# Performance work log

Measured on AMD Instinct MI355X. Metric: run time of the kernel, lower is better.

Reference implementation:

```python
import jax, jax.numpy as jnp
import numpy as np

B, L, H, N = 4, 4096, 1024, 16
EPS = 1e-6  # layer_norm_epsilon


def setup_inputs() -> dict:
    key = jax.random.key(0)
    ks = jax.random.split(key, 8)
    hidden_states = jax.random.normal(ks[0], (B, L, H), dtype=jnp.float32)
    attention_mask = jnp.ones((B, L), dtype=jnp.float32)
    norm_weight = jnp.ones((H,), dtype=jnp.float32)
    # S4D init: dt log-uniform in [1e-3, 1e-1]; S4D-Lin A init; random C, D
    dt_min, dt_max = 1e-3, 1e-1
    log_dt = jax.random.uniform(ks[1], (H,), dtype=jnp.float32) * (
        float(np.log(dt_max)) - float(np.log(dt_min))) + float(np.log(dt_min))
    log_A_real = jnp.log(0.5 * jnp.ones((H, N), dtype=jnp.float32))
    A_imag = jnp.broadcast_to(float(np.pi) * jnp.arange(N, dtype=jnp.float32), (H, N))
    C_real = jax.random.normal(ks[2], (H, N), dtype=jnp.float32) * (0.5 ** 0.5)
    C_imag = jax.random.normal(ks[3], (H, N), dtype=jnp.float32) * (0.5 ** 0.5)
    D = jax.random.normal(ks[4], (H,), dtype=jnp.float32)
    out_w = jax.random.normal(ks[5], (2 * H, H), dtype=jnp.float32) * 0.02  # 1x1 conv to 2H (GLU)
    out_b = jnp.zeros((2 * H,), dtype=jnp.float32)
    return dict(hidden_states=hidden_states, attention_mask=attention_mask,
                norm_weight=norm_weight, log_dt=log_dt, log_A_real=log_A_real,
                A_imag=A_imag, C_real=C_real, C_imag=C_imag, D=D,
                out_w=out_w, out_b=out_b)


def _s4d_kernel(log_dt, log_A_real, A_imag, C_real, C_imag, length):
    """Diagonal SSM convolution kernel k[h, l] (S4D ZOH discretization)."""
    dt = jnp.exp(log_dt)                                   # (H,)
    A = -jnp.exp(log_A_real) + 1j * A_imag                 # (H, N) complex64
    C = C_real + 1j * C_imag                               # (H, N)
    dtA = A * dt[:, None]                                  # (H, N)
    C_disc = C * (jnp.exp(dtA) - 1.0) / A                  # (H, N)
    vand = jnp.exp(dtA[:, :, None] * jnp.arange(length, dtype=jnp.float32))  # (H, N, L)
    k = 2.0 * jnp.einsum('hn,hnl->hl', C_disc, vand).real  # (H, L)
    return k.astype(jnp.float32)


def reference(hidden_states, attention_mask, norm_weight, log_dt, log_A_real,
              A_imag, C_real, C_imag, D, out_w, out_b):
    # LongT5LayerNorm: RMSNorm (no mean subtraction), variance in fp32
    var = jnp.mean(jnp.square(hidden_states.astype(jnp.float32)), axis=-1, keepdims=True)
    normed = hidden_states * jax.lax.rsqrt(var + EPS) * norm_weight  # (B, L, H)
    # mask padded positions, go to channel-major layout (B, H, L)
    u = (normed * attention_mask[..., None]).transpose(0, 2, 1)
    Lx = u.shape[-1]
    k = _s4d_kernel(log_dt, log_A_real, A_imag, C_real, C_imag, Lx)  # (H, L)
    # causal convolution via FFT of length 2L
    nfft = 2 * Lx
    k_f = jnp.fft.rfft(k, n=nfft)                 # (H, nfft//2+1)
    u_f = jnp.fft.rfft(u, n=nfft)                 # (B, H, nfft//2+1)
    y = jnp.fft.irfft(u_f * k_f, n=nfft)[..., :Lx]  # (B, H, L)
    y = y + u * D[:, None]                        # skip connection
    y = jax.nn.gelu(y, approximate=False)         # torch nn.GELU (exact)
    # output 1x1 conv to 2H, then GLU over the channel dim
    z = jnp.einsum('bhl,oh->bol', y, out_w) + out_b[:, None]
    a, b = jnp.split(z, 2, axis=1)
    ssm_out = (a * jax.nn.sigmoid(b)).transpose(0, 2, 1)  # (B, L, H)
    # residual + dropout (eval mode -> identity)
    return hidden_states + ssm_out
```

## Files before the change

### kernel.cpp

```cpp
#include <hip/hip_runtime.h>

#define B_   4
#define L_   4096
#define H_   1024
#define N_   16
#define CH_  64
#define NC_  (L_/CH_)
#define M_   (B_*L_)
#define O2_  (2*H_)
#define EPS_ 1e-6f

typedef __attribute__((ext_vector_type(4))) float  f32x4;
typedef __attribute__((ext_vector_type(8))) __bf16 bf16x8;

__device__ __forceinline__ unsigned short f2bf(float x) {
  union { float f; unsigned int u; } v; v.f = x;
  unsigned int r = v.u + 0x7FFFu + ((v.u >> 16) & 1u);
  return (unsigned short)(r >> 16);
}
__device__ __forceinline__ float bf2f(unsigned short x) {
  union { unsigned int u; float f; } v; v.u = ((unsigned int)x) << 16;
  return v.f;
}

__device__ __forceinline__ void async_copy16(const void* g, void* l) {
  __builtin_amdgcn_global_load_lds(
      (const __attribute__((address_space(1))) unsigned int*)g,
      (__attribute__((address_space(3))) unsigned int*)l, 16, 0, 0);
}

__global__ void k_prep(const float* __restrict__ log_dt,
                       const float* __restrict__ log_A_real,
                       const float* __restrict__ A_imag,
                       const float* __restrict__ C_real,
                       const float* __restrict__ C_imag,
                       const float* __restrict__ outw,
                       const float* __restrict__ outb,
                       float* __restrict__ wr,  float* __restrict__ wi,
                       float* __restrict__ c2r, float* __restrict__ c2i,
                       float* __restrict__ wpr, float* __restrict__ wpi,
                       unsigned short* __restrict__ Wbf,
                       float* __restrict__ bp) {
  int idx = blockIdx.x * 256 + threadIdx.x;
  int p = idx >> 10, hh = idx & (H_ - 1);
  size_t src = (size_t)((p >> 1) + (p & 1) * H_) * H_ + hh;
  Wbf[idx] = f2bf(outw[src]);
  if (idx < O2_) bp[idx] = outb[(idx >> 1) + (idx & 1) * H_];
  if (idx < H_ * N_) {
    int h = idx / N_, n = idx % N_;
    int hn = h * N_ + n;
    float dt  = expf(log_dt[h]);
    float Ar  = -expf(log_A_real[hn]);
    float Ai  = A_imag[hn];
    float dr  = Ar * dt, di = Ai * dt;
    float er  = expf(dr);
    float wrv = er * cosf(di), wiv = er * sinf(di);
    float e1r = wrv - 1.0f, e1i = wiv;
    float den = Ar * Ar + Ai * Ai;
    float qr  = (e1r * Ar + e1i * Ai) / den;
    float qi  = (e1i * Ar - e1r * Ai) / den;
    float Cr  = C_real[hn], Ci = C_imag[hn];
    float cdr = Cr * qr - Ci * qi;
    float cdi = Cr * qi + Ci * qr;
    float ep  = expf((float)CH_ * dr);
    int o = n * H_ + h;
    wr[o]  = wrv;  wi[o]  = wiv;
    c2r[o] = 2.0f * cdr; c2i[o] = 2.0f * cdi;
    wpr[o] = ep * cosf((float)CH_ * di);
    wpi[o] = ep * sinf((float)CH_ * di);
  }
}

__global__ __launch_bounds__(256) void k_scale(const float* __restrict__ hs,
                                               const float* __restrict__ mask,
                                               float* __restrict__ scale) {
  int m = blockIdx.x, tid = threadIdx.x;
  float4 v = reinterpret_cast<const float4*>(hs + (size_t)m * H_)[tid];
  float s = v.x * v.x + v.y * v.y + v.z * v.z + v.w * v.w;
  #pragma unroll
  for (int off = 32; off > 0; off >>= 1) s += __shfl_down(s, off, 64);
  __shared__ float ps[4];
  if ((tid & 63) == 0) ps[tid >> 6] = s;
  __syncthreads();
  if (tid == 0) {
    float var = (ps[0] + ps[1] + ps[2] + ps[3]) * (1.0f / H_);
    scale[m] = rsqrtf(var + EPS_) * mask[m];
  }
}

__global__ __launch_bounds__(256) void k_scan1(const float* __restrict__ hs,
                                               const float* __restrict__ nw,
                                               const float* __restrict__ scale,
                                               const float* __restrict__ wr_,
                                               const float* __restrict__ wi_,
                                               float* __restrict__ endr,
                                               float* __restrict__ endi,
                                               unsigned short* __restrict__ ubf) {
  int tid = threadIdx.x;
  int h = blockIdx.x * 256 + tid;
  int c = blockIdx.y, b = blockIdx.z;
  float wr[N_], wi[N_], xr[N_], xi[N_];
  #pragma unroll
  for (int n = 0; n < N_; n++) {
    wr[n] = wr_[n * H_ + h]; wi[n] = wi_[n * H_ + h];
    xr[n] = 0.f; xi[n] = 0.f;
  }
  float nwh = nw[h];
  int l0 = c * CH_;
  const float* scp = scale + (size_t)b * L_ + l0;
  const float* hp = hs + ((size_t)b * L_ + l0) * H_ + h;
  unsigned short* up = ubf + ((size_t)b * L_ + l0) * H_ + h;
  #pragma unroll 8
  for (int l = 0; l < CH_; l++) {
    float u = hp[(size_t)l * H_] * scp[l] * nwh;
    unsigned short ub = f2bf(u);
    up[(size_t)l * H_] = ub;
    u = bf2f(ub);
    #pragma unroll
    for (int n = 0; n < N_; n++) {
      float oxr = xr[n];
      xr[n] = fmaf(wr[n], oxr, fmaf(-wi[n], xi[n], u));
      xi[n] = fmaf(wr[n], xi[n], wi[n] * oxr);
    }
  }
  size_t base = (((size_t)b * NC_ + c) * N_) * H_ + h;
  #pragma unroll
  for (int n = 0; n < N_; n++) {
    endr[base + (size_t)n * H_] = xr[n];
    endi[base + (size_t)n * H_] = xi[n];
  }
}

__global__ __launch_bounds__(256) void k_carry(const float* __restrict__ wpr_,
                                               const float* __restrict__ wpi_,
                                               const float* __restrict__ endr,
                                               const float* __restrict__ endi,
                                               float* __restrict__ carr,
                                               float* __restrict__ cari) {
  int idx = blockIdx.x * 256 + threadIdx.x;
  int h = idx & (H_ - 1);
  int n = (idx >> 10) & (N_ - 1);
  int b = idx >> 14;
  float wprv = wpr_[n * H_ + h], wpiv = wpi_[n * H_ + h];
  float sr = 0.f, si = 0.f;
  size_t cstride = (size_t)N_ * H_;
  size_t base = ((size_t)b * NC_) * cstride + (size_t)n * H_ + h;
  for (int c = 0; c < NC_; c++, base += cstride) {
    carr[base] = sr; cari[base] = si;
    float er = endr[base], ei = endi[base];
    float osr = sr;
    sr = fmaf(wprv, osr,  fmaf(-wpiv, si, er));
    si = fmaf(wprv, si, fmaf(wpiv, osr, ei));
  }
}

__global__ __launch_bounds__(256) void k_scan2(const unsigned short* __restrict__ ubf,
                                               const float* __restrict__ wr_,
                                               const float* __restrict__ wi_,
                                               const float* __restrict__ c2r_,
                                               const float* __restrict__ c2i_,
                                               const float* __restrict__ Dp,
                                               const float* __restrict__ carr,
                                               const float* __restrict__ cari,
                                               unsigned short* __restrict__ ybf) {
  __shared__ __align__(16) unsigned short us[CH_ * 256];
  int tid = threadIdx.x;
  int hb = blockIdx.x;
  int c = blockIdx.y, b = blockIdx.z;
  int h = hb * 256 + tid;
  int l0 = c * CH_;
  const unsigned short* usrc = ubf + ((size_t)b * L_ + l0) * H_ + hb * 256;
  #pragma unroll
  for (int i = 0; i < 8; i++) {
    int g = i * 256 + tid;
    int l = g >> 5, hq = (g & 31) * 8;
    async_copy16(usrc + (size_t)l * H_ + hq, &us[g * 8]);
  }
  __syncthreads();

  float yacc[CH_];
  float Dh = Dp[h];
  #pragma unroll
  for (int l = 0; l < CH_; l++)
    yacc[l] = Dh * bf2f(us[l * 256 + tid]);

  size_t base = (((size_t)b * NC_ + c) * N_) * H_ + h;
  for (int n = 0; n < N_; n++) {
    float wrv = wr_[n * H_ + h],  wiv = wi_[n * H_ + h];
    float crv = c2r_[n * H_ + h], civ = c2i_[n * H_ + h];
    float xr = carr[base + (size_t)n * H_];
    float xi = cari[base + (size_t)n * H_];
    #pragma unroll
    for (int l = 0; l < CH_; l++) {
      float u = bf2f(us[l * 256 + tid]);
      float oxr = xr;
      xr = fmaf(wrv, oxr, fmaf(-wiv, xi, u));
      xi = fmaf(wrv, xi, wiv * oxr);
      yacc[l] = fmaf(crv, xr, fmaf(-civ, xi, yacc[l]));
    }
  }
  unsigned short* yp = ybf + ((size_t)b * L_ + l0) * H_ + h;
  #pragma unroll
  for (int l = 0; l < CH_; l++) {
    float yv = yacc[l];
    float g = 0.5f * yv * (1.0f + erff(yv * 0.70710678118654752f));
    yp[(size_t)l * H_] = f2bf(g);
  }
}

#define BM2 256
#define BN2 256
#define NT2 16
#define GST 132
#define GEMM_LDS 131072

#define STAGE_A(buf, half, kt) do { \
  async_copy16(Ag + (size_t)(bm + rp0 + ((half) << 6)) * H_ + (kt) * 64 + ca0, \
               sA + (buf) * 32768 + ((half) << 13) + tid * 16); \
  async_copy16(Ag + (size_t)(bm + rp1 + 64 + ((half) << 6)) * H_ + (kt) * 64 + ca1, \
               sA + (buf) * 32768 + ((half) << 13) + 16384 + tid * 16); \
} while (0)

#define STAGE_B(buf, eo, kt) do { \
  async_copy16(Bg + (size_t)(bn + ((rp0 >> 5) << 6) + (rp0 & 31) + ((eo) << 5)) * H_ + (kt) * 64 + ca0, \
               sB + (buf) * 32768 + ((rp0 >> 5) << 13) + ((rp0 & 31) << 7) + ((eo) << 12) + (q0 << 4)); \
  async_copy16(Bg + (size_t)(bn + ((rp1 >> 5) << 6) + (rp1 & 31) + ((eo) << 5)) * H_ + (kt) * 64 + ca1, \
               sB + (buf) * 32768 + ((rp1 >> 5) << 13) + ((rp1 & 31) << 7) + ((eo) << 12) + (q0 << 4)); \
} while (0)

#define VM4  asm volatile("s_waitcnt vmcnt(4)" ::: "memory")
#define NOVM do {} while (0)
#define NOLOAD do {} while (0)

#define LOAD_A(buf, mh) do { \
  _Pragma("unroll") \
  for (int m2 = 0; m2 < 4; m2++) { \
    _Pragma("unroll") \
    for (int kk = 0; kk < 2; kk++) \
      afr[m2][kk] = *reinterpret_cast<const bf16x8*>( \
          sA + (buf) * 32768 + (((wm << 7) + ((mh) << 6) + (m2 << 4)) << 7) + aoff[kk]); \
  } \
} while (0)

#define LOAD_B(buf, nh, dst) do { \
  _Pragma("unroll") \
  for (int n2 = 0; n2 < 2; n2++) { \
    _Pragma("unroll") \
    for (int kk = 0; kk < 2; kk++) \
      dst[n2][kk] = *reinterpret_cast<const bf16x8*>( \
          sB + (buf) * 32768 + (((wn << 6) + ((nh) << 5) + (n2 << 4)) << 7) + aoff[kk]); \
  } \
} while (0)

#define PH(LOADS, STAGE_STMT, mh, nh, bfx, CLOSE_STMT) do { \
  LOADS; \
  STAGE_STMT; \
  asm volatile("" ::: "memory"); \
  __builtin_amdgcn_s_barrier(); \
  asm volatile("s_waitcnt lgkmcnt(0)" ::: "memory"); \
  __builtin_amdgcn_sched_barrier(0); \
  __builtin_amdgcn_s_setprio(1); \
  _Pragma("unroll") \
  for (int m2 = 0; m2 < 4; m2++) { \
    _Pragma("unroll") \
    for (int n2 = 0; n2 < 2; n2++) { \
      _Pragma("unroll") \
      for (int kk = 0; kk < 2; kk++) \
        acc[(mh) * 4 + m2][(nh) * 2 + n2] = __builtin_amdgcn_mfma_f32_16x16x32_bf16( \
            afr[m2][kk], bfx[n2][kk], acc[(mh) * 4 + m2][(nh) * 2 + n2], 0, 0, 0); \
    } \
  } \
  __builtin_amdgcn_s_setprio(0); \
  CLOSE_STMT; \
  asm volatile("" ::: "memory"); \
  __builtin_amdgcn_s_barrier(); \
  asm volatile("" ::: "memory"); \
} while (0)

__global__ __launch_bounds__(512, 2) void k_gemm(const unsigned short* __restrict__ Ag,
                                                 const unsigned short* __restrict__ Bg,
                                                 const float* __restrict__ bp,
                                                 const float* __restrict__ hs,
                                                 float* __restrict__ out) {
  extern __shared__ __align__(16) char smem[];
  char* sA = smem;
  char* sB = smem + 65536;
  const int tid  = threadIdx.x;
  const int lane = tid & 63;
  const int wave = tid >> 6;
  const int wm = wave >> 2;
  const int wn = wave & 3;
  const int lin = blockIdx.y * 8 + blockIdx.x;
  const int w   = ((lin & 7) << 6) + (lin >> 3);
  const int bn  = (w & 7) * BN2;
  const int bm  = (w >> 3) * BM2;
  const int ar = lane & 15, kqi = lane >> 4;

  const int rp0 = tid >> 3, q0 = tid & 7;
  const int rp1 = rp0 + 64;
  const int ca0 = (q0 ^ (rp0 & 7)) * 8;
  const int ca1 = (q0 ^ (rp1 & 7)) * 8;
  int aoff[2];
  #pragma unroll
  for (int kk = 0; kk < 2; kk++)
    aoff[kk] = ar * 128 + (((kk * 4 + kqi) ^ (ar & 7)) << 4);

  f32x4 acc[8][4];
  #pragma unroll
  for (int mi = 0; mi < 8; mi++)
    #pragma unroll
    for (int ni = 0; ni < 4; ni++) acc[mi][ni] = (f32x4){0.f, 0.f, 0.f, 0.f};

  bf16x8 afr[4][2], bf0[2][2], bf1[2][2];

  STAGE_A(0, 0, 0);
  STAGE_B(0, 0, 0);
  STAGE_A(0, 1, 0);
  STAGE_B(0, 1, 0);
  STAGE_A(1, 0, 1);
  STAGE_B(1, 1, 1);
  VM4;
  __builtin_amdgcn_s_barrier();
  asm volatile("" ::: "memory");

  #pragma unroll 1
  for (int i = 0; i < NT2 / 2; i++) {
    const int tb = 2 * i + 1;
    const int tc = (2 * i + 2 < NT2) ? 2 * i + 2 : NT2 - 1;
    const int td = (2 * i + 3 < NT2) ? 2 * i + 3 : NT2 - 1;
    PH(LOAD_A(0, 0); LOAD_B(0, 0, bf0), STAGE_A(1, 1, tb), 0, 0, bf0, NOVM);
    PH(LOAD_B(0, 1, bf1),               STAGE_B(1, 0, tb), 0, 1, bf1, NOVM);
    PH(LOAD_A(0, 1),                    STAGE_A(0, 0, tc), 1, 1, bf1, NOVM);
    PH(NOLOAD,                          STAGE_B(0, 1, tc), 1, 0, bf0, VM4);
    PH(LOAD_A(1, 0); LOAD_B(1, 0, bf0), STAGE_A(0, 1, tc), 0, 0, bf0, NOVM);
    PH(LOAD_B(1, 1, bf1),               STAGE_B(0, 0, tc), 0, 1, bf1, NOVM);
    PH(LOAD_A(1, 1),                    STAGE_A(1, 0, td), 1, 1, bf1, NOVM);
    PH(NOLOAD,                          STAGE_B(1, 1, td), 1, 0, bf0, VM4);
  }
  asm volatile("s_waitcnt vmcnt(0)" ::: "memory");
  __builtin_amdgcn_s_barrier();
  asm volatile("" ::: "memory");

  float* gt = (float*)smem;
  #pragma unroll
  for (int hf = 0; hf < 2; hf++) {
    if (wm == hf) {
      #pragma unroll
      for (int ni = 0; ni < 4; ni++) {
        int p  = wn * 64 + ni * 16 + (lane & 15);
        int pe = (bn + p) & ~1;
        float bA = bp[pe], bB = bp[pe + 1];
        int jl = p >> 1;
        #pragma unroll
        for (int mi = 0; mi < 8; mi++) {
          int lrow0 = mi * 16 + (lane >> 4) * 4;
          #pragma unroll
          for (int r = 0; r < 4; r++) {
            float v = acc[mi][ni][r];
            float w2 = __shfl_xor(v, 1, 64);
            if (!(lane & 1))
              gt[(lrow0 + r) * GST + jl] = (v + bA) / (1.0f + __expf(-(w2 + bB)));
          }
        }
      }
    }
    __syncthreads();
    {
      const int c4 = tid & 31;
      const int rw = tid >> 5;
      const size_t obase = (size_t)(bm + hf * 128) * H_ + (bn >> 1);
      #pragma unroll
      for (int rep = 0; rep < 8; rep++) {
        int row = rep * 16 + rw;
        float4 g = *reinterpret_cast<const float4*>(&gt[row * GST + c4 * 4]);
        size_t o = obase + (size_t)row * H_ + c4 * 4;
        float4 hv = *reinterpret_cast<const float4*>(&hs[o]);
        float4 rv = {hv.x + g.x, hv.y + g.y, hv.z + g.z, hv.w + g.w};
        *reinterpret_cast<float4*>(&out[o]) = rv;
      }
    }
    __syncthreads();
  }
}

extern "C" void kernel_launch(void* const* d_in, const int* in_sizes, int n_in,
                              void* d_out, int out_size, void* d_ws, size_t ws_size,
                              hipStream_t stream) {
  const float* hs    = (const float*)d_in[0];
  const float* mask  = (const float*)d_in[1];
  const float* nw    = (const float*)d_in[2];
  const float* ldt   = (const float*)d_in[3];
  const float* lar   = (const float*)d_in[4];
  const float* aim   = (const float*)d_in[5];
  const float* crl   = (const float*)d_in[6];
  const float* cim   = (const float*)d_in[7];
  const float* Dp    = (const float*)d_in[8];
  const float* outw  = (const float*)d_in[9];
  const float* outb  = (const float*)d_in[10];
  float* out = (float*)d_out;

  static bool attr_done = false;
  if (!attr_done) {
    hipFuncSetAttribute((const void*)k_gemm,
                        hipFuncAttributeMaxDynamicSharedMemorySize, GEMM_LDS);
    attr_done = true;
  }

  size_t off = 0;
  char* ws = (char*)d_ws;
  auto nxt = [&](size_t bytes) -> void* {
    void* p = ws + off; off += (bytes + 255) & ~(size_t)255; return p;
  };
  float* wr   = (float*)nxt(H_ * N_ * 4);
  float* wi   = (float*)nxt(H_ * N_ * 4);
  float* c2r  = (float*)nxt(H_ * N_ * 4);
  float* c2i  = (float*)nxt(H_ * N_ * 4);
  float* wpr  = (float*)nxt(H_ * N_ * 4);
  float* wpi  = (float*)nxt(H_ * N_ * 4);
  float* bpck = (float*)nxt(O2_ * 4);
  float* scale= (float*)nxt((size_t)M_ * 4);
  float* endr = (float*)nxt((size_t)B_ * NC_ * N_ * H_ * 4);
  float* endi = (float*)nxt((size_t)B_ * NC_ * N_ * H_ * 4);
  float* carr = (float*)nxt((size_t)B_ * NC_ * N_ * H_ * 4);
  float* cari = (float*)nxt((size_t)B_ * NC_ * N_ * H_ * 4);
  unsigned short* Wbf = (unsigned short*)nxt((size_t)O2_ * H_ * 2);
  unsigned short* ubf = (unsigned short*)nxt((size_t)M_ * H_ * 2);
  unsigned short* ybf = (unsigned short*)nxt((size_t)M_ * H_ * 2);

  k_prep<<<dim3(O2_ * H_ / 256), dim3(256), 0, stream>>>(ldt, lar, aim, crl, cim,
                                                         outw, outb,
                                                         wr, wi, c2r, c2i, wpr, wpi,
                                                         Wbf, bpck);
  k_scale<<<dim3(M_), dim3(256), 0, stream>>>(hs, mask, scale);
  k_scan1<<<dim3(H_ / 256, NC_, B_), dim3(256), 0, stream>>>(hs, nw, scale, wr, wi,
                                                             endr, endi, ubf);
  k_carry<<<dim3(B_ * N_ * H_ / 256), dim3(256), 0, stream>>>(wpr, wpi, endr, endi, carr, cari);
  k_scan2<<<dim3(H_ / 256, NC_, B_), dim3(256), 0, stream>>>(ubf, wr, wi, c2r, c2i,
                                                             Dp, carr, cari, ybf);
  k_gemm<<<dim3(O2_ / BN2, M_ / BM2), dim3(512), GEMM_LDS, stream>>>(ybf, Wbf, bpck, hs, out);
}
```

Measured before the change: 369.0 us.

## Restructure chunk scan to state-in-registers and halve GEMM pipeline phases

The chunk scan kernel no longer stages u through LDS. Each thread now keeps all 16 complex states in registers, walks the chunk along L once, and reads u and writes the GELU output directly per step, which removes the shared-memory staging and the 64-entry accumulator array. The GEMM main loop merges pairs of phases, loading all four B fragments at once and issuing two async stages per phase, so it needs half as many barriers. The risks are higher register pressure in both kernels and less overlap of loads with MFMA work.

```diff
diff --git a/kernel.cpp b/kernel.cpp
--- a/kernel.cpp
+++ b/kernel.cpp
@@ -163,47 +163,35 @@
                                                const float* __restrict__ carr,
                                                const float* __restrict__ cari,
                                                unsigned short* __restrict__ ybf) {
-  __shared__ __align__(16) unsigned short us[CH_ * 256];
   int tid = threadIdx.x;
   int hb = blockIdx.x;
   int c = blockIdx.y, b = blockIdx.z;
   int h = hb * 256 + tid;
   int l0 = c * CH_;
-  const unsigned short* usrc = ubf + ((size_t)b * L_ + l0) * H_ + hb * 256;
-  #pragma unroll
-  for (int i = 0; i < 8; i++) {
-    int g = i * 256 + tid;
-    int l = g >> 5, hq = (g & 31) * 8;
-    async_copy16(usrc + (size_t)l * H_ + hq, &us[g * 8]);
-  }
-  __syncthreads();
-
-  float yacc[CH_];
+  float wrv[N_], wiv[N_], crv[N_], civ[N_], xr[N_], xi[N_];
+  size_t base = (((size_t)b * NC_ + c) * N_) * H_ + h;
+  #pragma unroll
+  for (int n = 0; n < N_; n++) {
+    wrv[n] = wr_[n * H_ + h];  wiv[n] = wi_[n * H_ + h];
+    crv[n] = c2r_[n * H_ + h]; civ[n] = c2i_[n * H_ + h];
+    xr[n]  = carr[base + (size_t)n * H_];
+    xi[n]  = cari[base + (size_t)n * H_];
+  }
   float Dh = Dp[h];
-  #pragma unroll
-  for (int l = 0; l < CH_; l++)
-    yacc[l] = Dh * bf2f(us[l * 256 + tid]);
-
-  size_t base = (((size_t)b * NC_ + c) * N_) * H_ + h;
-  for (int n = 0; n < N_; n++) {
-    float wrv = wr_[n * H_ + h],  wiv = wi_[n * H_ + h];
-    float crv = c2r_[n * H_ + h], civ = c2i_[n * H_ + h];
-    float xr = carr[base + (size_t)n * H_];
-    float xi = cari[base + (size_t)n * H_];
+  const unsigned short* up = ubf + ((size_t)b * L_ + l0) * H_ + h;
+  unsigned short* yp = ybf + ((size_t)b * L_ + l0) * H_ + h;
+  #pragma unroll 4
+  for (int l = 0; l < CH_; l++) {
+    float u = bf2f(up[(size_t)l * H_]);
+    float y = Dh * u;
     #pragma unroll
-    for (int l = 0; l < CH_; l++) {
-      float u = bf2f(us[l * 256 + tid]);
-      float oxr = xr;
-      xr = fmaf(wrv, oxr, fmaf(-wiv, xi, u));
-      xi = fmaf(wrv, xi, wiv * oxr);
-      yacc[l] = fmaf(crv, xr, fmaf(-civ, xi, yacc[l]));
+    for (int n = 0; n < N_; n++) {
+      float oxr = xr[n];
+      xr[n] = fmaf(wrv[n], oxr, fmaf(-wiv[n], xi[n], u));
+      xi[n] = fmaf(wrv[n], xi[n], wiv[n] * oxr);
+      y = fmaf(crv[n], xr[n], fmaf(-civ[n], xi[n], y));
     }
-  }
-  unsigned short* yp = ybf + ((size_t)b * L_ + l0) * H_ + h;
-  #pragma unroll
-  for (int l = 0; l < CH_; l++) {
-    float yv = yacc[l];
-    float g = 0.5f * yv * (1.0f + erff(yv * 0.70710678118654752f));
+    float g = 0.5f * y * (1.0f + erff(y * 0.70710678118654752f));
     yp[(size_t)l * H_] = f2bf(g);
   }
 }
@@ -230,7 +218,6 @@
 
 #define VM4  asm volatile("s_waitcnt vmcnt(4)" ::: "memory")
 #define NOVM do {} while (0)
-#define NOLOAD do {} while (0)
 
 #define LOAD_A(buf, mh) do { \
   _Pragma("unroll") \
@@ -242,19 +229,20 @@
   } \
 } while (0)
 
-#define LOAD_B(buf, nh, dst) do { \
+#define LOAD_B2(buf) do { \
   _Pragma("unroll") \
-  for (int n2 = 0; n2 < 2; n2++) { \
+  for (int n2 = 0; n2 < 4; n2++) { \
     _Pragma("unroll") \
     for (int kk = 0; kk < 2; kk++) \
-      dst[n2][kk] = *reinterpret_cast<const bf16x8*>( \
-          sB + (buf) * 32768 + (((wn << 6) + ((nh) << 5) + (n2 << 4)) << 7) + aoff[kk]); \
+      bfr[n2][kk] = *reinterpret_cast<const bf16x8*>( \
+          sB + (buf) * 32768 + (((wn << 6) + (n2 << 4)) << 7) + aoff[kk]); \
   } \
 } while (0)
 
-#define PH(LOADS, STAGE_STMT, mh, nh, bfx, CLOSE_STMT) do { \
+#define PH2(mh, LOADS, STAGE1, STAGE2, CLOSE_STMT) do { \
   LOADS; \
-  STAGE_STMT; \
+  STAGE1; \
+  STAGE2; \
   asm volatile("" ::: "memory"); \
   __builtin_amdgcn_s_barrier(); \
   asm volatile("s_waitcnt lgkmcnt(0)" ::: "memory"); \
@@ -263,11 +251,11 @@
   _Pragma("unroll") \
   for (int m2 = 0; m2 < 4; m2++) { \
     _Pragma("unroll") \
-    for (int n2 = 0; n2 < 2; n2++) { \
+    for (int n2 = 0; n2 < 4; n2++) { \
       _Pragma("unroll") \
       for (int kk = 0; kk < 2; kk++) \
-        acc[(mh) * 4 + m2][(nh) * 2 + n2] = __builtin_amdgcn_mfma_f32_16x16x32_bf16( \
-            afr[m2][kk], bfx[n2][kk], acc[(mh) * 4 + m2][(nh) * 2 + n2], 0, 0, 0); \
+        acc[(mh) * 4 + m2][n2] = __builtin_amdgcn_mfma_f32_16x16x32_bf16( \
+            afr[m2][kk], bfr[n2][kk], acc[(mh) * 4 + m2][n2], 0, 0, 0); \
     } \
   } \
   __builtin_amdgcn_s_setprio(0); \
@@ -311,7 +299,7 @@
     #pragma unroll
     for (int ni = 0; ni < 4; ni++) acc[mi][ni] = (f32x4){0.f, 0.f, 0.f, 0.f};
 
-  bf16x8 afr[4][2], bf0[2][2], bf1[2][2];
+  bf16x8 afr[4][2], bfr[4][2];
 
   STAGE_A(0, 0, 0);
   STAGE_B(0, 0, 0);
@@ -328,14 +316,10 @@
     const int tb = 2 * i + 1;
     const int tc = (2 * i + 2 < NT2) ? 2 * i + 2 : NT2 - 1;
     const int td = (2 * i + 3 < NT2) ? 2 * i + 3 : NT2 - 1;
-    PH(LOAD_A(0, 0); LOAD_B(0, 0, bf0), STAGE_A(1, 1, tb), 0, 0, bf0, NOVM);
-    PH(LOAD_B(0, 1, bf1),               STAGE_B(1, 0, tb), 0, 1, bf1, NOVM);
-    PH(LOAD_A(0, 1),                    STAGE_A(0, 0, tc), 1, 1, bf1, NOVM);
-    PH(NOLOAD,                          STAGE_B(0, 1, tc), 1, 0, bf0, VM4);
-    PH(LOAD_A(1, 0); LOAD_B(1, 0, bf0), STAGE_A(0, 1, tc), 0, 0, bf0, NOVM);
-    PH(LOAD_B(1, 1, bf1),               STAGE_B(0, 0, tc), 0, 1, bf1, NOVM);
-    PH(LOAD_A(1, 1),                    STAGE_A(1, 0, td), 1, 1, bf1, NOVM);
-    PH(NOLOAD,                          STAGE_B(1, 1, td), 1, 0, bf0, VM4);
+    PH2(0, LOAD_A(0, 0); LOAD_B2(0), STAGE_A(1, 1, tb), STAGE_B(1, 0, tb), NOVM);
+    PH2(1, LOAD_A(0, 1),             STAGE_A(0, 0, tc), STAGE_B(0, 1, tc), VM4);
+    PH2(0, LOAD_A(1, 0); LOAD_B2(1), STAGE_A(0, 1, tc), STAGE_B(0, 0, tc), NOVM);
+    PH2(1, LOAD_A(1, 1),             STAGE_A(1, 0, td), STAGE_B(1, 1, td), VM4);
   }
   asm volatile("s_waitcnt vmcnt(0)" ::: "memory");
   __builtin_amdgcn_s_barrier();
```

Measured after the change: 369.7 us. No clear change (+0.2%).
